# Performance work log

Hardware: AMD Instinct MI355X
Metric: run time of the kernel (lower is better)

## Reference

```python
import jax, jax.numpy as jnp
import numpy as np

HIDDEN = 2048
HEADS = 16
HEAD_DIM = HIDDEN // HEADS
B, L = 4, 2048


def _rotate_half(x):
    x1, x2 = jnp.split(x, 2, axis=-1)
    return jnp.concatenate([-x2, x1], axis=-1)


def setup_inputs() -> dict:
    key = jax.random.key(0)
    k1, k2, k3 = jax.random.split(key, 3)
    x = jax.random.normal(k1, (B, L, HIDDEN), dtype=jnp.float32)
    # realistic rotary tables
    inv_freq = 1.0 / (10000.0 ** (jnp.arange(0, HEAD_DIM, 2, dtype=jnp.float32) / HEAD_DIM))
    t = jnp.arange(L, dtype=jnp.float32)
    freqs = jnp.outer(t, inv_freq)  # [L, HEAD_DIM/2]
    emb = jnp.concatenate([freqs, freqs], axis=-1)  # [L, HEAD_DIM]
    cos = jnp.cos(emb)
    sin = jnp.sin(emb)
    w_qkv = jax.random.normal(k2, (3 * HIDDEN, HIDDEN), dtype=jnp.float32) * (HIDDEN ** -0.5)
    w_out = jax.random.normal(k3, (HIDDEN, HIDDEN), dtype=jnp.float32) * (HIDDEN ** -0.5)
    return {"x": x, "cos": cos, "sin": sin, "w_qkv": w_qkv, "w_out": w_out}


def reference(x, cos, sin, w_qkv, w_out):
    b, l, d = x.shape
    qkv = jnp.einsum('bld,ed->ble', x, w_qkv)  # [B, L, 3D]
    q, k, v = jnp.split(qkv, 3, axis=-1)
    # [B, H, L, Dh]
    q = q.reshape(b, l, HEADS, HEAD_DIM).transpose(0, 2, 1, 3)
    k = k.reshape(b, l, HEADS, HEAD_DIM).transpose(0, 2, 1, 3)
    v = v.reshape(b, l, HEADS, HEAD_DIM).transpose(0, 2, 1, 3)
    cos_ = cos[None, None, :l, :]
    sin_ = sin[None, None, :l, :]
    q = q * cos_ + _rotate_half(q) * sin_
    k = k * cos_ + _rotate_half(k) * sin_
    scale = 1.0 / jnp.sqrt(jnp.asarray(HEAD_DIM, dtype=q.dtype))
    scores = jnp.einsum('bhqd,bhkd->bhqk', q, k) * scale
    attn = jax.nn.softmax(scores, axis=-1)
    out = jnp.einsum('bhqk,bhkd->bhqd', attn, v)  # [B, H, L, Dh]
    out = out.transpose(0, 2, 1, 3).reshape(b, l, d)
    return jnp.einsum('bld,ed->ble', out, w_out)
```

## Files before the change

### kernel.cpp

```cpp
#include <hip/hip_runtime.h>
#include <cstdint>
#include <cstddef>

typedef unsigned short u16;
typedef __attribute__((ext_vector_type(8))) short bf16x8;
typedef __attribute__((ext_vector_type(4))) float f32x4;

#define DEVFN static __device__ __forceinline__

DEVFN u16 f2bf(float f) {
  unsigned u = __float_as_uint(f);
  unsigned r = (u + 0x7FFFu + ((u >> 16) & 1u)) >> 16;
  return (u16)r;
}

DEVFN void gload16(const void* g, void* l) {
  __builtin_amdgcn_global_load_lds(
      (const __attribute__((address_space(1))) void*)g,
      (__attribute__((address_space(3))) void*)l, 16, 0, 0);
}

__global__ void prep(const float* __restrict__ x, const float* __restrict__ wqkv,
                     const float* __restrict__ wout, const float* __restrict__ cosp,
                     const float* __restrict__ sinp, u16* __restrict__ xb,
                     u16* __restrict__ wqkvb, u16* __restrict__ woutb,
                     float2* __restrict__ cs) {
  constexpr int X4 = 4194304;
  constexpr int W4 = 3145728;
  constexpr int O4 = 1048576;
  int i = blockIdx.x * blockDim.x + threadIdx.x;
  if (i < X4) {
    float4 v = ((const float4*)x)[i];
    unsigned long long w = (unsigned long long)f2bf(v.x)
        | ((unsigned long long)f2bf(v.y) << 16)
        | ((unsigned long long)f2bf(v.z) << 32)
        | ((unsigned long long)f2bf(v.w) << 48);
    *(unsigned long long*)(xb + (size_t)i * 4) = w;
  } else if (i < X4 + W4) {
    int j = i - X4;
    int base = j * 4;
    int e = base >> 11, col = base & 2047;
    int e2;
    if (e < 4096) {
      int part = e >> 11, loc = e & 2047;
      int h = loc >> 7, d = loc & 127;
      int d2 = (d < 64) ? 2 * d : 2 * (d - 64) + 1;
      e2 = part * 2048 + h * 128 + d2;
    } else {
      e2 = e;
    }
    float4 v = *(const float4*)&wqkv[(size_t)base];
    unsigned long long w = (unsigned long long)f2bf(v.x)
        | ((unsigned long long)f2bf(v.y) << 16)
        | ((unsigned long long)f2bf(v.z) << 32)
        | ((unsigned long long)f2bf(v.w) << 48);
    *(unsigned long long*)(wqkvb + (size_t)e2 * 2048 + col) = w;
  } else if (i < X4 + W4 + O4) {
    int j = i - X4 - W4;
    float4 v = ((const float4*)wout)[j];
    unsigned long long w = (unsigned long long)f2bf(v.x)
        | ((unsigned long long)f2bf(v.y) << 16)
        | ((unsigned long long)f2bf(v.z) << 32)
        | ((unsigned long long)f2bf(v.w) << 48);
    *(unsigned long long*)(woutb + (size_t)j * 4) = w;
  } else {
    int k = i - X4 - W4 - O4;
    int ld4 = k * 4;
#pragma unroll
    for (int u = 0; u < 4; u++) {
      int ld = ld4 + u;
      int l = ld >> 6, d = ld & 63;
      cs[ld] = make_float2(cosp[(size_t)l * 128 + d], sinp[(size_t)l * 128 + d]);
    }
  }
}

enum { M_F32OUT = 0, M_ROPE = 1, M_VT = 2 };

template <int MODE>
DEVFN void gemm_core(const u16* __restrict__ A, const u16* __restrict__ Bt,
                     void* __restrict__ Cv, const float2* __restrict__ cs,
                     int N, int K, int m0, int n0, u16* As, u16* Bs) {
  int tid = threadIdx.x;
  int wv = tid >> 6, lane = tid & 63, quad = lane >> 4, l16 = lane & 15;
  int wm = (wv >> 1) * 64, wn = (wv & 1) * 64;
  f32x4 acc[4][4] = {};
  int r0 = wv * 16 + (lane >> 2);
  int r1 = r0 + 64;
  int c0 = (lane & 3) ^ ((r0 >> 1) & 3);
  int c1 = (lane & 3) ^ ((r1 >> 1) & 3);
  const u16* Ap0 = A + (size_t)(m0 + r0) * K + c0 * 8;
  const u16* Ap1 = A + (size_t)(m0 + r1) * K + c1 * 8;
  const u16* Bp0 = Bt + (size_t)(n0 + r0) * K + c0 * 8;
  const u16* Bp1 = Bt + (size_t)(n0 + r1) * K + c1 * 8;
  u16* As0 = &As[(wv * 16) * 32];
  u16* As1 = &As[(wv * 16 + 64) * 32];
  u16* Bs0 = &Bs[(wv * 16) * 32];
  u16* Bs1 = &Bs[(wv * 16 + 64) * 32];
  for (int k0 = 0; k0 < K; k0 += 32) {
    __syncthreads();
    gload16(Ap0, As0);
    gload16(Ap1, As1);
    gload16(Bp0, Bs0);
    gload16(Bp1, Bs1);
    Ap0 += 32; Ap1 += 32; Bp0 += 32; Bp1 += 32;
    __syncthreads();
    bf16x8 af[4], bf[4];
#pragma unroll
    for (int i = 0; i < 4; i++) {
      int r = wm + i * 16 + l16;
      af[i] = *(const bf16x8*)&As[r * 32 + ((quad ^ ((r >> 1) & 3)) << 3)];
    }
#pragma unroll
    for (int j = 0; j < 4; j++) {
      int r = wn + j * 16 + l16;
      bf[j] = *(const bf16x8*)&Bs[r * 32 + ((quad ^ ((r >> 1) & 3)) << 3)];
    }
#pragma unroll
    for (int i = 0; i < 4; i++)
#pragma unroll
      for (int j = 0; j < 4; j++) {
        if (MODE == M_VT)
          acc[i][j] = __builtin_amdgcn_mfma_f32_16x16x32_bf16(bf[j], af[i], acc[i][j], 0, 0, 0);
        else
          acc[i][j] = __builtin_amdgcn_mfma_f32_16x16x32_bf16(af[i], bf[j], acc[i][j], 0, 0, 0);
      }
  }
  if (MODE == M_F32OUT) {
    float* C = (float*)Cv;
#pragma unroll
    for (int i = 0; i < 4; i++)
#pragma unroll
      for (int r = 0; r < 4; r++) {
        size_t row = (size_t)(m0 + wm + i * 16 + quad * 4 + r);
#pragma unroll
        for (int j = 0; j < 4; j++)
          C[row * N + (n0 + wn + j * 16 + l16)] = acc[i][j][r];
      }
  } else if (MODE == M_ROPE) {
    constexpr float QSCALE = 1.4426950408889634f * 0.08838834764831845f;
    const float scale = (n0 >> 11) ? 1.0f : QSCALE;
    u16* C = (u16*)Cv;
#pragma unroll
    for (int i = 0; i < 4; i++)
#pragma unroll
      for (int r = 0; r < 4; r++) {
        int row = m0 + wm + i * 16 + quad * 4 + r;
        int l = row & 2047;
#pragma unroll
        for (int j = 0; j < 4; j++) {
          int col = n0 + wn + j * 16 + l16;
          int dm = (col & 127) >> 1;
          float2 csv = cs[l * 64 + dm];
          float v = acc[i][j][r];
          float pv = __shfl_xor(v, 1);
          float sg = (l16 & 1) ? csv.y : -csv.y;
          C[(size_t)row * 4096 + col] = f2bf((v * csv.x + pv * sg) * scale);
        }
      }
  } else {
    u16* vt = (u16*)Cv;
#pragma unroll
    for (int j = 0; j < 4; j++)
#pragma unroll
      for (int r = 0; r < 4; r++) {
        int vch = n0 + wn + j * 16 + quad * 4 + r;
        int h = vch >> 7, d = vch & 127;
#pragma unroll
        for (int i = 0; i < 4; i++) {
          int token = m0 + wm + i * 16 + l16;
          int b = token >> 11, lloc = token & 2047;
          vt[((size_t)(b * 16 + h)) * 262144 + (size_t)d * 2048 + lloc] =
              f2bf(acc[i][j][r]);
        }
      }
  }
}

__global__ __launch_bounds__(256) void gemm_qkv(const u16* __restrict__ xb,
                                                const u16* __restrict__ wqkvb,
                                                u16* __restrict__ qkvo,
                                                u16* __restrict__ vto,
                                                const float2* __restrict__ cs) {
  __shared__ u16 As[128 * 32];
  __shared__ u16 Bs[128 * 32];
  int id = blockIdx.x;
  int xcd = id & 7, sub = id >> 3;
  int bx = sub % 48, by = xcd * 8 + sub / 48;
  if (bx < 32)
    gemm_core<M_ROPE>(xb, wqkvb, qkvo, cs, 0, 2048, by * 128, bx * 128, As, Bs);
  else
    gemm_core<M_VT>(xb, wqkvb + (size_t)4096 * 2048, vto, nullptr, 0, 2048,
                    by * 128, (bx - 32) * 128, As, Bs);
}

__global__ __launch_bounds__(256) void gemm_out_k(const u16* __restrict__ A,
                                                  const u16* __restrict__ Bt,
                                                  float* __restrict__ C) {
  __shared__ u16 As[128 * 32];
  __shared__ u16 Bs[128 * 32];
  int id = blockIdx.x;
  int xcd = id & 7, sub = id >> 3;
  int bx = sub % 16, by = xcd * 8 + sub / 16;
  gemm_core<M_F32OUT>(A, Bt, C, nullptr, 2048, 2048, by * 128, bx * 128, As, Bs);
}

DEVFN int swz(int row, int chunk)   { return row * 128 + ((chunk ^ (row & 15)) << 3); }
DEVFN int swz64(int row, int chunk) { return row * 64  + ((chunk ^ (row & 7)) << 3); }

__global__ __launch_bounds__(512) void attn_fused(const u16* __restrict__ qkv,
                                                  const u16* __restrict__ vt,
                                                  u16* __restrict__ out) {
  __shared__ u16 S[40960];
  u16* const Pb = S + 32768;
  int tid = threadIdx.x;
  int wv = tid >> 6, lane = tid & 63, quad = lane >> 4, l16 = lane & 15;
  int id = blockIdx.x;
  int xcd = id & 7, sub = id >> 3;
  int bh = ((sub >> 4) << 3) | xcd;
  int qt = sub & 15;
  int b = bh >> 4, h = bh & 15;
  const u16* qptr = qkv + (size_t)b * 2048 * 4096 + h * 128;
  const u16* kptr = qptr + 2048;
  const u16* vptr = vt + (size_t)bh * 262144;
  int q0 = qt * 128;

#pragma unroll
  for (int j = 0; j < 4; j++) {
    int rb = wv * 4 + j * 32;
    int r = rb + (lane >> 4);
    int ck = (lane & 15) ^ (r & 15);
    gload16(&qptr[(size_t)(q0 + r) * 4096 + ck * 8], &S[rb * 128]);
  }
  __syncthreads();
  bf16x8 qf[4];
#pragma unroll
  for (int ks = 0; ks < 4; ks++)
    qf[ks] = *(const bf16x8*)&S[swz(wv * 16 + l16, ks * 4 + quad)];
  __syncthreads();

  f32x4 o[8] = {};
  float l[4] = {0.f, 0.f, 0.f, 0.f};

#pragma unroll
  for (int j = 0; j < 2; j++) {
    int rbk = wv * 4 + j * 32;
    int rk = rbk + (lane >> 4);
    int ckk = (lane & 15) ^ (rk & 15);
    gload16(&kptr[(size_t)rk * 4096 + ckk * 8], &S[rbk * 128]);
    int rbv = wv * 8 + j * 64;
    int rv = rbv + (lane >> 3);
    int ckv = (lane & 7) ^ (rv & 7);
    gload16(&vptr[(size_t)rv * 2048 + ckv * 8], &S[16384 + rbv * 64]);
  }

  for (int kt = 0; kt < 32; kt++) {
    int cur = kt & 1;
    const u16* Kc = S + cur * 8192;
    const u16* Vc = S + 16384 + cur * 8192;
    __syncthreads();
    if (kt < 31) {
      int kk0 = (kt + 1) * 64;
      u16* kb = S + (cur ^ 1) * 8192;
      u16* vb = S + 16384 + (cur ^ 1) * 8192;
#pragma unroll
      for (int j = 0; j < 2; j++) {
        int rbk = wv * 4 + j * 32;
        int rk = rbk + (lane >> 4);
        int ckk = (lane & 15) ^ (rk & 15);
        gload16(&kptr[(size_t)(kk0 + rk) * 4096 + ckk * 8], &kb[rbk * 128]);
        int rbv = wv * 8 + j * 64;
        int rv = rbv + (lane >> 3);
        int ckv = (lane & 7) ^ (rv & 7);
        gload16(&vptr[(size_t)rv * 2048 + kk0 + ckv * 8], &vb[rbv * 64]);
      }
    }
    f32x4 s[4] = {};
#pragma unroll
    for (int ks = 0; ks < 4; ks++) {
#pragma unroll
      for (int nt = 0; nt < 4; nt++) {
        bf16x8 bfr = *(const bf16x8*)&Kc[swz(nt * 16 + l16, ks * 4 + quad)];
        s[nt] = __builtin_amdgcn_mfma_f32_16x16x32_bf16(qf[ks], bfr, s[nt], 0, 0, 0);
      }
    }
#pragma unroll
    for (int nt = 0; nt < 4; nt++)
#pragma unroll
      for (int r = 0; r < 4; r++) {
        float p = exp2f(s[nt][r]);
        l[r] += p;
        int row = wv * 16 + quad * 4 + r;
        int col = nt * 16 + l16;
        Pb[swz64(row, col >> 3) + (col & 7)] = f2bf(p);
      }
#pragma unroll
    for (int ks = 0; ks < 2; ks++) {
      bf16x8 pf = *(const bf16x8*)&Pb[swz64(wv * 16 + l16, ks * 4 + quad)];
#pragma unroll
      for (int nt = 0; nt < 8; nt++) {
        bf16x8 vf = *(const bf16x8*)&Vc[swz64(nt * 16 + l16, ks * 4 + quad)];
        o[nt] = __builtin_amdgcn_mfma_f32_16x16x32_bf16(pf, vf, o[nt], 0, 0, 0);
      }
    }
  }
#pragma unroll
  for (int r = 0; r < 4; r++)
#pragma unroll
    for (int off = 1; off < 16; off <<= 1) l[r] += __shfl_xor(l[r], off, 16);
  u16* obase = out + ((size_t)b * 2048 + q0) * 2048 + h * 128;
#pragma unroll
  for (int r = 0; r < 4; r++) {
    float inv = 1.0f / l[r];
    int row = wv * 16 + quad * 4 + r;
#pragma unroll
    for (int nt = 0; nt < 8; nt++)
      obase[(size_t)row * 2048 + nt * 16 + l16] = f2bf(o[nt][r] * inv);
  }
}

extern "C" void kernel_launch(void* const* d_in, const int* in_sizes, int n_in,
                              void* d_out, int out_size, void* d_ws, size_t ws_size,
                              hipStream_t stream) {
  const float* x    = (const float*)d_in[0];
  const float* cosp = (const float*)d_in[1];
  const float* sinp = (const float*)d_in[2];
  const float* wqkv = (const float*)d_in[3];
  const float* wout = (const float*)d_in[4];
  float* outp = (float*)d_out;

  u16* ws    = (u16*)d_ws;
  u16* xb    = ws;
  u16* wqkvb = xb + 16777216;
  u16* woutb = wqkvb + 12582912;
  u16* qkv   = woutb + 4194304;
  u16* vt    = qkv + 33554432;
  float2* cs = (float2*)(vt + 16777216);
  u16* attn  = xb;

  prep<<<32896, 256, 0, stream>>>(x, wqkv, wout, cosp, sinp, xb, wqkvb, woutb, cs);
  gemm_qkv<<<3072, 256, 0, stream>>>(xb, wqkvb, qkv, vt, cs);
  attn_fused<<<1024, 512, 0, stream>>>(qkv, vt, attn);
  gemm_out_k<<<1024, 256, 0, stream>>>(attn, woutb, outp);
}
```

Baseline: 707.2 us.

## Rewrite projection GEMMs as 256x256 tiles with double-buffered async LDS pipeline

Replaces the 128x128, K=32 single-buffered GEMM core used by the QKV and output projections with a 256x256 tile and K=64 step run by 512 threads. Global-to-LDS loads for the next K slice are split into four stages, each interleaved with one quarter of the MFMA work and gated by explicit vmcnt waits and barriers, with raised wave priority around the MFMA bursts. The aim is to increase data reuse per tile and hide global load latency behind matrix math. The cost is 128KB of LDS per block and many more accumulator registers, which may limit occupancy, and the grids shrink to 768 and 256 blocks, which may leave some compute units underused.

```diff
diff --git a/kernel.cpp b/kernel.cpp
--- a/kernel.cpp
+++ b/kernel.cpp
@@ -19,6 +19,11 @@
       (const __attribute__((address_space(1))) void*)g,
       (__attribute__((address_space(3))) void*)l, 16, 0, 0);
 }
+
+#define WAITVM(n) asm volatile("s_waitcnt vmcnt(" #n ")" ::: "memory")
+#define BARRIER() do { asm volatile("" ::: "memory"); \
+                       __builtin_amdgcn_s_barrier();   \
+                       asm volatile("" ::: "memory"); } while (0)
 
 __global__ void prep(const float* __restrict__ x, const float* __restrict__ wqkv,
                      const float* __restrict__ wout, const float* __restrict__ cosp,
@@ -77,79 +82,148 @@
 
 enum { M_F32OUT = 0, M_ROPE = 1, M_VT = 2 };
 
+DEVFN bf16x8 rdfrag(const u16* buf, int row, int chunk) {
+  return *(const bf16x8*)&buf[row * 64 + (((chunk ^ (row & 7)) & 7) << 3)];
+}
+
+template <int MODE, int Q>
+DEVFN void phase_mfma(const u16* Ac, const u16* Bc, int wm, int wn, int quad, int l16,
+                      bf16x8 (&bfr)[4][2], f32x4 (&acc)[8][4]) {
+  if (Q == 0) {
+#pragma unroll
+    for (int j = 0; j < 4; j++)
+#pragma unroll
+      for (int kk = 0; kk < 2; kk++)
+        bfr[j][kk] = rdfrag(Bc, wn * 64 + j * 16 + l16, kk * 4 + quad);
+  }
+  bf16x8 af[2][2];
+#pragma unroll
+  for (int i2 = 0; i2 < 2; i2++)
+#pragma unroll
+    for (int kk = 0; kk < 2; kk++)
+      af[i2][kk] = rdfrag(Ac, wm * 128 + (Q * 2 + i2) * 16 + l16, kk * 4 + quad);
+  __builtin_amdgcn_s_setprio(1);
+#pragma unroll
+  for (int kk = 0; kk < 2; kk++)
+#pragma unroll
+    for (int i2 = 0; i2 < 2; i2++)
+#pragma unroll
+      for (int j = 0; j < 4; j++) {
+        if (MODE == M_VT)
+          acc[Q * 2 + i2][j] = __builtin_amdgcn_mfma_f32_16x16x32_bf16(
+              bfr[j][kk], af[i2][kk], acc[Q * 2 + i2][j], 0, 0, 0);
+        else
+          acc[Q * 2 + i2][j] = __builtin_amdgcn_mfma_f32_16x16x32_bf16(
+              af[i2][kk], bfr[j][kk], acc[Q * 2 + i2][j], 0, 0, 0);
+      }
+  __builtin_amdgcn_s_setprio(0);
+}
+
 template <int MODE>
-DEVFN void gemm_core(const u16* __restrict__ A, const u16* __restrict__ Bt,
-                     void* __restrict__ Cv, const float2* __restrict__ cs,
-                     int N, int K, int m0, int n0, u16* As, u16* Bs) {
+DEVFN void gemm256_core(const u16* __restrict__ A, const u16* __restrict__ Bt,
+                        void* __restrict__ Cv, const float2* __restrict__ cs,
+                        int N, int m0, int n0, u16* As, u16* Bs) {
   int tid = threadIdx.x;
   int wv = tid >> 6, lane = tid & 63, quad = lane >> 4, l16 = lane & 15;
-  int wm = (wv >> 1) * 64, wn = (wv & 1) * 64;
-  f32x4 acc[4][4] = {};
-  int r0 = wv * 16 + (lane >> 2);
-  int r1 = r0 + 64;
-  int c0 = (lane & 3) ^ ((r0 >> 1) & 3);
-  int c1 = (lane & 3) ^ ((r1 >> 1) & 3);
-  const u16* Ap0 = A + (size_t)(m0 + r0) * K + c0 * 8;
-  const u16* Ap1 = A + (size_t)(m0 + r1) * K + c1 * 8;
-  const u16* Bp0 = Bt + (size_t)(n0 + r0) * K + c0 * 8;
-  const u16* Bp1 = Bt + (size_t)(n0 + r1) * K + c1 * 8;
-  u16* As0 = &As[(wv * 16) * 32];
-  u16* As1 = &As[(wv * 16 + 64) * 32];
-  u16* Bs0 = &Bs[(wv * 16) * 32];
-  u16* Bs1 = &Bs[(wv * 16 + 64) * 32];
-  for (int k0 = 0; k0 < K; k0 += 32) {
-    __syncthreads();
-    gload16(Ap0, As0);
-    gload16(Ap1, As1);
-    gload16(Bp0, Bs0);
-    gload16(Bp1, Bs1);
-    Ap0 += 32; Ap1 += 32; Bp0 += 32; Bp1 += 32;
-    __syncthreads();
-    bf16x8 af[4], bf[4];
-#pragma unroll
-    for (int i = 0; i < 4; i++) {
-      int r = wm + i * 16 + l16;
-      af[i] = *(const bf16x8*)&As[r * 32 + ((quad ^ ((r >> 1) & 3)) << 3)];
-    }
-#pragma unroll
-    for (int j = 0; j < 4; j++) {
-      int r = wn + j * 16 + l16;
-      bf[j] = *(const bf16x8*)&Bs[r * 32 + ((quad ^ ((r >> 1) & 3)) << 3)];
-    }
-#pragma unroll
-    for (int i = 0; i < 4; i++)
-#pragma unroll
-      for (int j = 0; j < 4; j++) {
-        if (MODE == M_VT)
-          acc[i][j] = __builtin_amdgcn_mfma_f32_16x16x32_bf16(bf[j], af[i], acc[i][j], 0, 0, 0);
-        else
-          acc[i][j] = __builtin_amdgcn_mfma_f32_16x16x32_bf16(af[i], bf[j], acc[i][j], 0, 0, 0);
-      }
-  }
+  int wm = wv >> 2, wn = wv & 3;
+
+  const u16* pB[2][2];
+  const u16* pA[4];
+#pragma unroll
+  for (int h = 0; h < 2; h++)
+#pragma unroll
+    for (int o = 0; o < 2; o++) {
+      int r = h * 128 + o * 64 + wv * 8 + (lane >> 3);
+      int ck = (lane & 7) ^ (r & 7);
+      pB[h][o] = Bt + (size_t)(n0 + r) * 2048 + ck * 8;
+    }
+#pragma unroll
+  for (int q = 0; q < 4; q++) {
+    int rb = (wv < 4) ? (q * 32 + wv * 8) : (128 + q * 32 + (wv - 4) * 8);
+    int r = rb + (lane >> 3);
+    int ck = (lane & 7) ^ (r & 7);
+    pA[q] = A + (size_t)(m0 + r) * 2048 + ck * 8;
+  }
+
+#define STAGE_B(h, buf, kk) do {                                    \
+    int rb0_ = (h) * 128 + wv * 8;                                  \
+    gload16(pB[h][0] + (kk), &(buf)[rb0_ * 64]);                    \
+    gload16(pB[h][1] + (kk), &(buf)[(rb0_ + 64) * 64]); } while (0)
+#define STAGE_A(q, buf, kk) do {                                    \
+    int rb_ = ((wv < 4) ? ((q) * 32 + wv * 8)                       \
+                        : (128 + (q) * 32 + (wv - 4) * 8));         \
+    gload16(pA[q] + (kk), &(buf)[rb_ * 64]); } while (0)
+
+  f32x4 acc[8][4] = {};
+  bf16x8 bfr[4][2];
+
+  STAGE_B(0, Bs, 0);
+  STAGE_B(1, Bs, 0);
+  STAGE_A(0, As, 0);
+  STAGE_A(1, As, 0);
+  STAGE_A(2, As, 0);
+  STAGE_A(3, As, 0);
+
+  for (int t = 0; t < 31; t++) {
+    const u16* Ac = As + (t & 1) * 16384;
+    const u16* Bc = Bs + (t & 1) * 16384;
+    u16* An = As + ((t + 1) & 1) * 16384;
+    u16* Bn = Bs + ((t + 1) & 1) * 16384;
+    int kn = (t + 1) * 64;
+    STAGE_B(0, Bn, kn);
+    WAITVM(5); BARRIER();
+    phase_mfma<MODE, 0>(Ac, Bc, wm, wn, quad, l16, bfr, acc);
+    STAGE_B(1, Bn, kn);
+    WAITVM(6); BARRIER();
+    phase_mfma<MODE, 1>(Ac, Bc, wm, wn, quad, l16, bfr, acc);
+    STAGE_A(0, An, kn);
+    STAGE_A(1, An, kn);
+    WAITVM(7); BARRIER();
+    phase_mfma<MODE, 2>(Ac, Bc, wm, wn, quad, l16, bfr, acc);
+    STAGE_A(2, An, kn);
+    STAGE_A(3, An, kn);
+    WAITVM(8); BARRIER();
+    phase_mfma<MODE, 3>(Ac, Bc, wm, wn, quad, l16, bfr, acc);
+  }
+  {
+    const u16* Ac = As + 16384;
+    const u16* Bc = Bs + 16384;
+    WAITVM(3); BARRIER();
+    phase_mfma<MODE, 0>(Ac, Bc, wm, wn, quad, l16, bfr, acc);
+    WAITVM(2); BARRIER();
+    phase_mfma<MODE, 1>(Ac, Bc, wm, wn, quad, l16, bfr, acc);
+    WAITVM(1); BARRIER();
+    phase_mfma<MODE, 2>(Ac, Bc, wm, wn, quad, l16, bfr, acc);
+    WAITVM(0); BARRIER();
+    phase_mfma<MODE, 3>(Ac, Bc, wm, wn, quad, l16, bfr, acc);
+  }
+#undef STAGE_B
+#undef STAGE_A
+
   if (MODE == M_F32OUT) {
     float* C = (float*)Cv;
 #pragma unroll
-    for (int i = 0; i < 4; i++)
+    for (int i = 0; i < 8; i++)
 #pragma unroll
       for (int r = 0; r < 4; r++) {
-        size_t row = (size_t)(m0 + wm + i * 16 + quad * 4 + r);
+        size_t row = (size_t)(m0 + wm * 128 + i * 16 + quad * 4 + r);
 #pragma unroll
         for (int j = 0; j < 4; j++)
-          C[row * N + (n0 + wn + j * 16 + l16)] = acc[i][j][r];
+          C[row * N + (n0 + wn * 64 + j * 16 + l16)] = acc[i][j][r];
       }
   } else if (MODE == M_ROPE) {
     constexpr float QSCALE = 1.4426950408889634f * 0.08838834764831845f;
     const float scale = (n0 >> 11) ? 1.0f : QSCALE;
     u16* C = (u16*)Cv;
 #pragma unroll
-    for (int i = 0; i < 4; i++)
+    for (int i = 0; i < 8; i++)
 #pragma unroll
       for (int r = 0; r < 4; r++) {
-        int row = m0 + wm + i * 16 + quad * 4 + r;
+        int row = m0 + wm * 128 + i * 16 + quad * 4 + r;
         int l = row & 2047;
 #pragma unroll
         for (int j = 0; j < 4; j++) {
-          int col = n0 + wn + j * 16 + l16;
+          int col = n0 + wn * 64 + j * 16 + l16;
           int dm = (col & 127) >> 1;
           float2 csv = cs[l * 64 + dm];
           float v = acc[i][j][r];
@@ -164,11 +238,11 @@
     for (int j = 0; j < 4; j++)
 #pragma unroll
       for (int r = 0; r < 4; r++) {
-        int vch = n0 + wn + j * 16 + quad * 4 + r;
+        int vch = n0 + wn * 64 + j * 16 + quad * 4 + r;
         int h = vch >> 7, d = vch & 127;
 #pragma unroll
-        for (int i = 0; i < 4; i++) {
-          int token = m0 + wm + i * 16 + l16;
+        for (int i = 0; i < 8; i++) {
+          int token = m0 + wm * 128 + i * 16 + l16;
           int b = token >> 11, lloc = token & 2047;
           vt[((size_t)(b * 16 + h)) * 262144 + (size_t)d * 2048 + lloc] =
               f2bf(acc[i][j][r]);
@@ -177,32 +251,32 @@
   }
 }
 
-__global__ __launch_bounds__(256) void gemm_qkv(const u16* __restrict__ xb,
-                                                const u16* __restrict__ wqkvb,
-                                                u16* __restrict__ qkvo,
-                                                u16* __restrict__ vto,
-                                                const float2* __restrict__ cs) {
-  __shared__ u16 As[128 * 32];
-  __shared__ u16 Bs[128 * 32];
+__global__ __launch_bounds__(512, 2) void gemm_qkv(const u16* __restrict__ xb,
+                                                   const u16* __restrict__ wqkvb,
+                                                   u16* __restrict__ qkvo,
+                                                   u16* __restrict__ vto,
+                                                   const float2* __restrict__ cs) {
+  __shared__ u16 As[32768];
+  __shared__ u16 Bs[32768];
   int id = blockIdx.x;
   int xcd = id & 7, sub = id >> 3;
-  int bx = sub % 48, by = xcd * 8 + sub / 48;
-  if (bx < 32)
-    gemm_core<M_ROPE>(xb, wqkvb, qkvo, cs, 0, 2048, by * 128, bx * 128, As, Bs);
+  int bx = sub % 24, by = xcd * 4 + sub / 24;
+  if (bx < 16)
+    gemm256_core<M_ROPE>(xb, wqkvb, qkvo, cs, 0, by * 256, bx * 256, As, Bs);
   else
-    gemm_core<M_VT>(xb, wqkvb + (size_t)4096 * 2048, vto, nullptr, 0, 2048,
-                    by * 128, (bx - 32) * 128, As, Bs);
-}
-
-__global__ __launch_bounds__(256) void gemm_out_k(const u16* __restrict__ A,
-                                                  const u16* __restrict__ Bt,
-                                                  float* __restrict__ C) {
-  __shared__ u16 As[128 * 32];
-  __shared__ u16 Bs[128 * 32];
+    gemm256_core<M_VT>(xb, wqkvb + (size_t)4096 * 2048, vto, nullptr, 0,
+                       by * 256, (bx - 16) * 256, As, Bs);
+}
+
+__global__ __launch_bounds__(512, 2) void gemm_out_k(const u16* __restrict__ A,
+                                                     const u16* __restrict__ Bt,
+                                                     float* __restrict__ C) {
+  __shared__ u16 As[32768];
+  __shared__ u16 Bs[32768];
   int id = blockIdx.x;
   int xcd = id & 7, sub = id >> 3;
-  int bx = sub % 16, by = xcd * 8 + sub / 16;
-  gemm_core<M_F32OUT>(A, Bt, C, nullptr, 2048, 2048, by * 128, bx * 128, As, Bs);
+  int bx = sub % 8, by = xcd * 4 + sub / 8;
+  gemm256_core<M_F32OUT>(A, Bt, C, nullptr, 2048, by * 256, bx * 256, As, Bs);
 }
 
 DEVFN int swz(int row, int chunk)   { return row * 128 + ((chunk ^ (row & 15)) << 3); }
@@ -339,7 +413,7 @@
   u16* attn  = xb;
 
   prep<<<32896, 256, 0, stream>>>(x, wqkv, wout, cosp, sinp, xb, wqkvb, woutb, cs);
-  gemm_qkv<<<3072, 256, 0, stream>>>(xb, wqkvb, qkv, vt, cs);
+  gemm_qkv<<<768, 512, 0, stream>>>(xb, wqkvb, qkv, vt, cs);
   attn_fused<<<1024, 512, 0, stream>>>(qkv, vt, attn);
-  gemm_out_k<<<1024, 256, 0, stream>>>(attn, woutb, outp);
-}
+  gemm_out_k<<<256, 512, 0, stream>>>(attn, woutb, outp);
+}
```

Result: faster. 664.4 us (-6.1%).
